# Optimization experiments

Hardware: AMD Instinct MI355X
Metric: run time of the kernel (lower is better)

## Reference

```python
import jax, jax.numpy as jnp
import numpy as np

N = 50000      # nodes
E = 800000     # edges
IN = 128       # in_dim
H = 8          # heads
C = 16         # h_dim (per-head out channels)
ED = 16        # edge_dim
G = 1000       # number of graphs
HC = H * C     # 128
EPS = 1e-16    # PyG softmax epsilon


def setup_inputs() -> dict:
    key = jax.random.key(0)
    ks = jax.random.split(key, 32)
    p = lambda i, shape: jax.random.normal(ks[i], shape, jnp.float32) * 0.1
    inp = {
        "x": jax.random.normal(ks[0], (N, IN), jnp.float32),
        "edge_index": jax.random.randint(ks[1], (2, E), 0, N),
        "edge_attr": jax.random.normal(ks[2], (E, ED), jnp.float32),
        "batch": jnp.sort(jax.random.randint(ks[3], (N,), 0, G)),
    }
    dims = [IN, HC, HC]
    for l in range(3):
        d = dims[l]
        inp[f"W{l+1}"] = p(4 + 6 * l, (d, HC))     # lin weight
        inp[f"We{l+1}"] = p(5 + 6 * l, (ED, HC))   # lin_edge weight
        inp[f"as{l+1}"] = p(6 + 6 * l, (H, C))     # att_src
        inp[f"ad{l+1}"] = p(7 + 6 * l, (H, C))     # att_dst
        inp[f"ae{l+1}"] = p(8 + 6 * l, (H, C))     # att_edge
        inp[f"b{l+1}"] = jnp.zeros((HC,), jnp.float32)
    D = 4 * HC  # cat(h1,h2,h3,h_pool_) -> 512
    inp["Wl1"] = p(22, (D, D)); inp["bl1"] = jnp.zeros((D,), jnp.float32)
    inp["Wl2"] = p(23, (D, 1)); inp["bl2"] = jnp.zeros((1,), jnp.float32)
    return inp


def gat_conv(x, src, dst, edge_attr, W, We, a_s, a_d, a_e, b):
    # x: [N, d_in] -> xs: [N, H, C]
    xs = (x @ W).reshape(-1, H, C)
    ea = (edge_attr @ We).reshape(-1, H, C)          # [E, H, C]
    al_src = jnp.sum(xs * a_s, axis=-1)              # [N, H]
    al_dst = jnp.sum(xs * a_d, axis=-1)              # [N, H]
    al_e = jnp.sum(ea * a_e, axis=-1)                # [E, H]
    alpha = al_src[src] + al_dst[dst] + al_e         # [E, H]
    alpha = jax.nn.leaky_relu(alpha, 0.2)
    amax = jax.ops.segment_max(alpha, dst, num_segments=N)
    ex = jnp.exp(alpha - amax[dst])
    denom = jax.ops.segment_sum(ex, dst, num_segments=N)
    alpha = ex / (denom[dst] + EPS)                  # softmax over in-edges of dst
    msg = xs[src] * alpha[..., None]                 # [E, H, C]
    out = jax.ops.segment_sum(msg, dst, num_segments=N)  # [N, H, C]
    return out.reshape(-1, HC) + b


def reference(x, edge_index, edge_attr, batch,
              W1, We1, as1, ad1, ae1, b1,
              W2, We2, as2, ad2, ae2, b2,
              W3, We3, as3, ad3, ae3, b3,
              Wl1, bl1, Wl2, bl2):
    src, dst = edge_index[0], edge_index[1]
    h1 = gat_conv(x, src, dst, edge_attr, W1, We1, as1, ad1, ae1, b1)
    h2 = gat_conv(h1, src, dst, edge_attr, W2, We2, as2, ad2, ae2, b2)
    h3 = gat_conv(h2, src, dst, edge_attr, W3, We3, as3, ad3, ae3, b3)
    # global_add_pool then broadcast back per node (vectorized gather,
    # replacing the original per-node python loop)
    h_pool = jax.ops.segment_sum(h3, batch, num_segments=G)   # [G, HC]
    h_pool_ = h_pool[batch]                                    # [N, HC]
    h = jnp.concatenate([h1, h2, h3, h_pool_], axis=1)         # [N, 4*HC]
    h = jax.nn.leaky_relu(h @ Wl1 + bl1, 0.01)
    return h @ Wl2 + bl2
```

## Files before the change

### kernel.cpp

```cpp
#include <hip/hip_runtime.h>

#define N_NODES 50000
#define N_EDGES 800000
#define N_GRAPH 1000
#define EPAD (N_EDGES + 8 * N_NODES)

typedef short bf16x8 __attribute__((ext_vector_type(8)));
typedef float f32x4 __attribute__((ext_vector_type(4)));

__device__ inline short f2b(float f) {
    union { float f; unsigned u; } x; x.f = f;
    unsigned r = x.u + 0x7FFF + ((x.u >> 16) & 1);
    return (short)(r >> 16);
}
__device__ inline float b2f_lo(unsigned v) {
    union { unsigned u; float f; } x; x.u = v << 16; return x.f;
}
__device__ inline float b2f_hi(unsigned v) {
    union { unsigned u; float f; } x; x.u = v & 0xFFFF0000u; return x.f;
}
__device__ inline float b2f_s(short s) {
    union { unsigned u; float f; } x; x.u = ((unsigned)(unsigned short)s) << 16; return x.f;
}
__device__ inline unsigned pack2(short lo, short hi) {
    return ((unsigned)(unsigned short)lo) | (((unsigned)(unsigned short)hi) << 16);
}

__global__ void f2b_bulk(const float* __restrict__ in, short* __restrict__ out, int n4) {
    int t = blockIdx.x * blockDim.x + threadIdx.x;
    if (t >= n4) return;
    float4 v = *(const float4*)(in + (size_t)t * 4);
    *(short4*)(out + (size_t)t * 4) = make_short4(f2b(v.x), f2b(v.y), f2b(v.z), f2b(v.w));
}

__global__ void wbt_k(const float* __restrict__ W, short* __restrict__ WbT) {
    int idx = blockIdx.x * blockDim.x + threadIdx.x;
    int k = idx >> 7, c = idx & 127;
    WbT[(size_t)c * 128 + k] = f2b(W[idx]);
}

__global__ __launch_bounds__(256) void gemm_mfma(const short* __restrict__ Ab,
                                                 const short* __restrict__ WbT,
                                                 short* __restrict__ outb, int nrows) {
    const int tid = threadIdx.x;
    const int n0 = blockIdx.x * 64;
    const int wid = tid >> 6, lane = tid & 63;
    const int lr = lane & 15, kg = lane >> 4;
    const int wr = (wid >> 1) * 32;
    const int wc = (wid & 1) * 64;

    f32x4 acc[2][4] = {};

#pragma unroll
    for (int ks = 0; ks < 4; ks++) {
        const int k0 = ks * 32;
        bf16x8 a[2], b[4];
#pragma unroll
        for (int fm = 0; fm < 2; fm++) {
            int gr = n0 + wr + fm * 16 + lr;
            bf16x8 v = {};
            if (gr < nrows) v = *(const bf16x8*)(Ab + (size_t)gr * 128 + k0 + kg * 8);
            a[fm] = v;
        }
#pragma unroll
        for (int fn = 0; fn < 4; fn++)
            b[fn] = *(const bf16x8*)(WbT + (size_t)(wc + fn * 16 + lr) * 128 + k0 + kg * 8);
#pragma unroll
        for (int fm = 0; fm < 2; fm++)
#pragma unroll
            for (int fn = 0; fn < 4; fn++)
                acc[fm][fn] = __builtin_amdgcn_mfma_f32_16x16x32_bf16(
                    a[fm], b[fn], acc[fm][fn], 0, 0, 0);
    }
#pragma unroll
    for (int fm = 0; fm < 2; fm++) {
#pragma unroll
        for (int r = 0; r < 4; r++) {
            int gr = n0 + wr + fm * 16 + kg * 4 + r;
            if (gr < nrows) {
#pragma unroll
                for (int fn = 0; fn < 4; fn++) {
                    int col = wc + fn * 16 + lr;
                    outb[(size_t)gr * 128 + col] = f2b(acc[fm][fn][r]);
                }
            }
        }
    }
}

__global__ void node_al(const short* __restrict__ xsb, const float* __restrict__ a_s,
                        const float* __restrict__ a_d, float* __restrict__ alsrc,
                        float* __restrict__ aldst, int n) {
    int t = blockIdx.x * blockDim.x + threadIdx.x;
    if (t >= n * 8) return;
    int node = t >> 3, h = t & 7;
    const short* xp = xsb + (size_t)node * 128 + h * 16;
    uint4 u0 = *(const uint4*)(xp);
    uint4 u1 = *(const uint4*)(xp + 8);
    unsigned w[8] = {u0.x, u0.y, u0.z, u0.w, u1.x, u1.y, u1.z, u1.w};
    float ss = 0.f, dd = 0.f;
#pragma unroll
    for (int q = 0; q < 8; q++) {
        float lo = b2f_lo(w[q]), hi = b2f_hi(w[q]);
        ss += lo * a_s[h * 16 + q * 2] + hi * a_s[h * 16 + q * 2 + 1];
        dd += lo * a_d[h * 16 + q * 2] + hi * a_d[h * 16 + q * 2 + 1];
    }
    alsrc[t] = ss;
    aldst[t] = dd;
}

__global__ void hist_k(const int* __restrict__ ei, int* __restrict__ cnt, int ne) {
    int e = blockIdx.x * blockDim.x + threadIdx.x;
    if (e < ne) atomicAdd(&cnt[ei[ne + e]], 1);
}

__global__ void scan1_k(const int* __restrict__ cnt, int* __restrict__ rowptr,
                        int* __restrict__ part, int n) {
    __shared__ int s[256];
    int tid = threadIdx.x;
    int i = blockIdx.x * 256 + tid;
    int v = (i < n) ? ((cnt[i] + 7) & ~7) : 0;
    s[tid] = v; __syncthreads();
#pragma unroll
    for (int off = 1; off < 256; off <<= 1) {
        int t = (tid >= off) ? s[tid - off] : 0;
        __syncthreads();
        s[tid] += t;
        __syncthreads();
    }
    if (i < n) rowptr[i] = s[tid] - v;
    if (tid == 255) part[blockIdx.x] = s[255];
}

__global__ void scan2_k(int* __restrict__ part, int npart) {
    __shared__ int s[256];
    int tid = threadIdx.x;
    int v = (tid < npart) ? part[tid] : 0;
    s[tid] = v; __syncthreads();
#pragma unroll
    for (int off = 1; off < 256; off <<= 1) {
        int t = (tid >= off) ? s[tid - off] : 0;
        __syncthreads();
        s[tid] += t;
        __syncthreads();
    }
    if (tid < npart) part[tid] = s[tid] - v;
}

__global__ void scan3_k(int* __restrict__ rowptr, const int* __restrict__ part,
                        const int* __restrict__ cnt, int* __restrict__ cursor, int n) {
    int i = blockIdx.x * 256 + threadIdx.x;
    if (i < n) {
        int r = rowptr[i] + part[blockIdx.x];
        rowptr[i] = r;
        cursor[i] = r;
        if (i == n - 1) rowptr[n] = r + ((cnt[i] + 7) & ~7);
    }
}

__global__ void scatter_k(const int* __restrict__ ei, const float* __restrict__ eattr,
                          int* __restrict__ cursor, int* __restrict__ csr_src,
                          short* __restrict__ eatb, int ne) {
    int e = blockIdx.x * blockDim.x + threadIdx.x;
    if (e >= ne) return;
    int d = ei[ne + e];
    int p = atomicAdd(&cursor[d], 1);
    csr_src[p] = ei[e];
    const float4* ep = (const float4*)(eattr + (size_t)e * 16);
    short* op = eatb + (size_t)p * 16;
#pragma unroll
    for (int q = 0; q < 4; q++) {
        float4 v = ep[q];
        *(short4*)(op + q * 4) = make_short4(f2b(v.x), f2b(v.y), f2b(v.z), f2b(v.w));
    }
}

__global__ __launch_bounds__(256) void ale_k(const int* __restrict__ csr_src,
                                             const short* __restrict__ eatb,
                                             const float* __restrict__ alsrc,
                                             const float* __restrict__ We,
                                             const float* __restrict__ ae,
                                             short* __restrict__ aleb, int ntot) {
    __shared__ float sAe[128];
    if (threadIdx.x < 128) {
        int k = threadIdx.x >> 3, h = threadIdx.x & 7;
        float s = 0.f;
#pragma unroll
        for (int c = 0; c < 16; c++) s += We[k * 128 + h * 16 + c] * ae[h * 16 + c];
        sAe[threadIdx.x] = s;
    }
    __syncthreads();
    int e = blockIdx.x * blockDim.x + threadIdx.x;
    if (e >= ntot) return;
    int s = csr_src[e];
    short* op = aleb + (size_t)e * 8;
    if (s < 0) {
        short m = f2b(-300.f);
        *(short4*)(op)     = make_short4(m, m, m, m);
        *(short4*)(op + 4) = make_short4(m, m, m, m);
        return;
    }
    uint4 u0 = *(const uint4*)(eatb + (size_t)e * 16);
    uint4 u1 = *(const uint4*)(eatb + (size_t)e * 16 + 8);
    unsigned w[8] = {u0.x, u0.y, u0.z, u0.w, u1.x, u1.y, u1.z, u1.w};
    float ea[16];
#pragma unroll
    for (int q = 0; q < 8; q++) { ea[q * 2] = b2f_lo(w[q]); ea[q * 2 + 1] = b2f_hi(w[q]); }
    float out[8];
    const float4* ap = (const float4*)(alsrc + (size_t)s * 8);
    float4 a0 = ap[0], a1 = ap[1];
    out[0] = a0.x; out[1] = a0.y; out[2] = a0.z; out[3] = a0.w;
    out[4] = a1.x; out[5] = a1.y; out[6] = a1.z; out[7] = a1.w;
#pragma unroll
    for (int k = 0; k < 16; k++)
#pragma unroll
        for (int h = 0; h < 8; h++) out[h] += ea[k] * sAe[k * 8 + h];
    short v8[8];
#pragma unroll
    for (int h = 0; h < 8; h++) v8[h] = f2b(out[h]);
    *(short4*)(op)     = make_short4(v8[0], v8[1], v8[2], v8[3]);
    *(short4*)(op + 4) = make_short4(v8[4], v8[5], v8[6], v8[7]);
}

__global__ __launch_bounds__(256) void gather_k(const int* __restrict__ rowptr,
                                                const int* __restrict__ csr_src,
                                                const short* __restrict__ aleb,
                                                const float* __restrict__ aldst,
                                                const short* __restrict__ xsb,
                                                const float* __restrict__ b,
                                                short* __restrict__ houtb, int n) {
    int dst = blockIdx.x * 4 + (threadIdx.x >> 6);
    if (dst >= n) return;
    const int lane = threadIdx.x & 63;
    const int h = lane >> 3;
    const float L2E = 1.44269504f;
    int p0 = rowptr[dst], p1 = rowptr[dst + 1];
    float ald = aldst[dst * 8 + h];
    float den = 0.f, acc0 = 0.f, acc1 = 0.f;
    const int nfull = (p1 - p0) >> 3;
    int p = p0;
    int   sv  = 0;
    float alv = 0.f;
    if (nfull > 0) {
        sv  = csr_src[p + (lane & 7)];
        alv = b2f_s(aleb[(size_t)p * 8 + lane]);
    }
    for (int c = 0; c < nfull; c++) {
        int csv = sv; float calv = alv;
        int pn = p + 8;
        if (c + 1 < nfull) {
            sv  = csr_src[pn + (lane & 7)];
            alv = b2f_s(aleb[(size_t)pn * 8 + lane]);
        }
        int s0 = __shfl(csv, 0), s1 = __shfl(csv, 1), s2 = __shfl(csv, 2), s3 = __shfl(csv, 3);
        int s4 = __shfl(csv, 4), s5 = __shfl(csv, 5), s6 = __shfl(csv, 6), s7 = __shfl(csv, 7);
        s0 = s0 < 0 ? 0 : s0;  s1 = s1 < 0 ? 0 : s1;
        s2 = s2 < 0 ? 0 : s2;  s3 = s3 < 0 ? 0 : s3;
        s4 = s4 < 0 ? 0 : s4;  s5 = s5 < 0 ? 0 : s5;
        s6 = s6 < 0 ? 0 : s6;  s7 = s7 < 0 ? 0 : s7;
        unsigned v0 = *(const unsigned*)(xsb + (size_t)s0 * 128 + lane * 2);
        unsigned v1 = *(const unsigned*)(xsb + (size_t)s1 * 128 + lane * 2);
        unsigned v2 = *(const unsigned*)(xsb + (size_t)s2 * 128 + lane * 2);
        unsigned v3 = *(const unsigned*)(xsb + (size_t)s3 * 128 + lane * 2);
        unsigned v4 = *(const unsigned*)(xsb + (size_t)s4 * 128 + lane * 2);
        unsigned v5 = *(const unsigned*)(xsb + (size_t)s5 * 128 + lane * 2);
        unsigned v6 = *(const unsigned*)(xsb + (size_t)s6 * 128 + lane * 2);
        unsigned v7 = *(const unsigned*)(xsb + (size_t)s7 * 128 + lane * 2);
        unsigned vv[8] = {v0, v1, v2, v3, v4, v5, v6, v7};
#pragma unroll
        for (int i = 0; i < 8; i++) {
            float al = __shfl(calv, i * 8 + h);
            float lg = al + ald; lg = lg > 0.f ? lg : 0.2f * lg;
            float ex = exp2f(lg * L2E);
            den  += ex;
            acc0 += b2f_lo(vv[i]) * ex;
            acc1 += b2f_hi(vv[i]) * ex;
        }
        p = pn;
    }
    float inv = 1.f / (den + 1e-16f);
    const float2 bb = *(const float2*)(b + lane * 2);
    unsigned o = pack2(f2b(acc0 * inv + bb.x), f2b(acc1 * inv + bb.y));
    *(unsigned*)(houtb + (size_t)dst * 128 + lane * 2) = o;
}

__global__ void pool_k(const short* __restrict__ h3b, const int* __restrict__ batch,
                       float* __restrict__ pool, int n) {
    int t = blockIdx.x * blockDim.x + threadIdx.x;
    if (t >= n * 128) return;
    int node = t >> 7, j = t & 127;
    atomicAdd(pool + (size_t)batch[node] * 128 + j, b2f_s(h3b[t]));
}

__global__ void wl1t_k(const float* __restrict__ Wl1, short* __restrict__ Wl1T) {
    int idx = blockIdx.x * blockDim.x + threadIdx.x;
    int k = idx >> 9, c = idx & 511;
    Wl1T[(size_t)c * 512 + k] = f2b(Wl1[idx]);
}

__global__ void init_out(float* __restrict__ out, const float* __restrict__ bl2, int n) {
    int t = blockIdx.x * blockDim.x + threadIdx.x;
    if (t < n) out[t] = bl2[0];
}

__global__ __launch_bounds__(256) void final_mfma(
    const short* __restrict__ h1, const short* __restrict__ h2,
    const short* __restrict__ h3, const short* __restrict__ poolb,
    const int* __restrict__ batch, const short* __restrict__ Wl1T,
    const float* __restrict__ bl1, const float* __restrict__ Wl2,
    float* __restrict__ out, int nrows)
{
    __shared__ short Abuf[2][4 * 64 * 8];
    __shared__ int   sBatch[64];
    const int tid = threadIdx.x;
    const int n0 = blockIdx.x * 64;
    const int j0 = blockIdx.y * 256;
    const int wid = tid >> 6, lane = tid & 63;
    const int lr = lane & 15, kg = lane >> 4;

    if (tid < 64) {
        int gr = n0 + tid;
        sBatch[tid] = (gr < nrows) ? batch[gr] : 0;
    }
    __syncthreads();

    const short* seg_base[4] = {h1, h2, h3, poolb};

    auto STAGE = [&](int t) {
        const int k0 = t * 32;
        const int seg = k0 >> 7;
        const short* base = seg_base[seg];
        const int cseg = k0 & 127;
        int gr = n0 + lane;
        int grow = (seg == 3) ? sBatch[lane] : ((gr < nrows) ? gr : 0);
        const short* src = base + (size_t)grow * 128 + cseg + wid * 8;
#if __has_builtin(__builtin_amdgcn_global_load_lds)
        __builtin_amdgcn_global_load_lds(
            (const __attribute__((address_space(1))) unsigned int*)src,
            (__attribute__((address_space(3))) unsigned int*)&Abuf[t & 1][(wid * 64 + lane) * 8],
            16, 0, 0);
#else
        uint4 v = *(const uint4*)src;
        *(uint4*)(&Abuf[t & 1][(wid * 64 + lane) * 8]) = v;
#endif
    };
    auto LOADB = [&](int t, bf16x8* bb) {
        const int k0 = t * 32;
#pragma unroll
        for (int fn = 0; fn < 4; fn++)
            bb[fn] = *(const bf16x8*)(Wl1T + (size_t)(j0 + wid * 64 + fn * 16 + lr) * 512
                                      + k0 + kg * 8);
    };

    f32x4 acc[4][4] = {};
    bf16x8 bc[4], bn[4];

    STAGE(0);
    LOADB(0, bc);
    __syncthreads();
#pragma unroll
    for (int t = 0; t < 16; t++) {
        if (t < 15) {
            STAGE(t + 1);
            LOADB(t + 1, bn);
        }
        bf16x8 a[4];
#pragma unroll
        for (int fm = 0; fm < 4; fm++)
            a[fm] = *(const bf16x8*)(&Abuf[t & 1][(kg * 64 + fm * 16 + lr) * 8]);
#pragma unroll
        for (int fm = 0; fm < 4; fm++)
#pragma unroll
            for (int fn = 0; fn < 4; fn++)
                acc[fm][fn] = __builtin_amdgcn_mfma_f32_16x16x32_bf16(
                    a[fm], bc[fn], acc[fm][fn], 0, 0, 0);
        if (t < 15) {
            __syncthreads();
#pragma unroll
            for (int fn = 0; fn < 4; fn++) bc[fn] = bn[fn];
        }
    }

    float w2[4], b1c[4];
#pragma unroll
    for (int fn = 0; fn < 4; fn++) {
        int c = j0 + wid * 64 + fn * 16 + lr;
        w2[fn]  = Wl2[c];
        b1c[fn] = bl1[c];
    }

#pragma unroll
    for (int fm = 0; fm < 4; fm++) {
#pragma unroll
        for (int r = 0; r < 4; r++) {
            float s = 0.f;
#pragma unroll
            for (int fn = 0; fn < 4; fn++) {
                float z = acc[fm][fn][r] + b1c[fn];
                z = z > 0.f ? z : 0.01f * z;
                s += z * w2[fn];
            }
            s += __shfl_xor(s, 1);
            s += __shfl_xor(s, 2);
            s += __shfl_xor(s, 4);
            s += __shfl_xor(s, 8);
            if (lr == 0) {
                int gr = n0 + fm * 16 + kg * 4 + r;
                if (gr < nrows) atomicAdd(out + gr, s);
            }
        }
    }
}

extern "C" void kernel_launch(void* const* d_in, const int* in_sizes, int n_in,
                              void* d_out, int out_size, void* d_ws, size_t ws_size,
                              hipStream_t stream) {
    const float* x     = (const float*)d_in[0];
    const int*   ei    = (const int*)d_in[1];
    const float* eattr = (const float*)d_in[2];
    const int*   batch = (const int*)d_in[3];
    const float* W[3]   = {(const float*)d_in[4],  (const float*)d_in[10], (const float*)d_in[16]};
    const float* We[3]  = {(const float*)d_in[5],  (const float*)d_in[11], (const float*)d_in[17]};
    const float* as_[3] = {(const float*)d_in[6],  (const float*)d_in[12], (const float*)d_in[18]};
    const float* ad_[3] = {(const float*)d_in[7],  (const float*)d_in[13], (const float*)d_in[19]};
    const float* ae_[3] = {(const float*)d_in[8],  (const float*)d_in[14], (const float*)d_in[20]};
    const float* b_[3]  = {(const float*)d_in[9],  (const float*)d_in[15], (const float*)d_in[21]};
    const float* Wl1 = (const float*)d_in[22];
    const float* bl1 = (const float*)d_in[23];
    const float* Wl2 = (const float*)d_in[24];
    const float* bl2 = (const float*)d_in[25];

    const int N = N_NODES, E = N_EDGES, G = N_GRAPH;

    float* ws    = (float*)d_ws;
    float* alsrc = ws;
    float* aldst = alsrc + (size_t)N * 8;
    float* pool  = aldst + (size_t)N * 8;
    short* xb    = (short*)(pool + (size_t)G * 128);
    short* xsb   = xb + (size_t)N * 128;
    short* hb0   = xsb + (size_t)N * 128;
    short* hb1   = hb0 + (size_t)N * 128;
    short* hb2   = hb1 + (size_t)N * 128;
    short* hb[3] = {hb0, hb1, hb2};
    short* poolb = hb2 + (size_t)N * 128;
    short* wbt0  = poolb + (size_t)G * 128;
    short* wbt1  = wbt0 + 16384;
    short* wbt2  = wbt1 + 16384;
    short* wbt[3] = {wbt0, wbt1, wbt2};
    short* wl1t  = wbt2 + 16384;
    short* aleb  = wl1t + 262144;
    short* eatb  = aleb + (size_t)EPAD * 8;
    int*   cnt     = (int*)(eatb + (size_t)EPAD * 16);
    int*   rowptr  = cnt + N;
    int*   cursor  = rowptr + N + 1;
    int*   part    = cursor + N;
    int*   csr_src = part + 256;

    f2b_bulk<<<(N * 32 + 255) / 256, 256, 0, stream>>>(x, xb, N * 32);
    for (int l = 0; l < 3; l++)
        wbt_k<<<64, 256, 0, stream>>>(W[l], wbt[l]);
    wl1t_k<<<1024, 256, 0, stream>>>(Wl1, wl1t);
    hipMemsetAsync(cnt, 0, (size_t)N * sizeof(int), stream);
    hipMemsetAsync(csr_src, 0x80, (size_t)EPAD * sizeof(int), stream);
    hist_k<<<(E + 255) / 256, 256, 0, stream>>>(ei, cnt, E);
    const int nblk = (N + 255) / 256;
    scan1_k<<<nblk, 256, 0, stream>>>(cnt, rowptr, part, N);
    scan2_k<<<1, 256, 0, stream>>>(part, nblk);
    scan3_k<<<nblk, 256, 0, stream>>>(rowptr, part, cnt, cursor, N);
    scatter_k<<<(E + 255) / 256, 256, 0, stream>>>(ei, eattr, cursor, csr_src, eatb, E);

    const int aleGrid = (EPAD + 255) / 256;
    for (int l = 0; l < 3; l++) {
        const short* Ain = (l == 0) ? xb : hb[l - 1];
        gemm_mfma<<<(N + 63) / 64, 256, 0, stream>>>(Ain, wbt[l], xsb, N);
        node_al<<<(N * 8 + 255) / 256, 256, 0, stream>>>(xsb, as_[l], ad_[l], alsrc, aldst, N);
        ale_k<<<aleGrid, 256, 0, stream>>>(csr_src, eatb, alsrc, We[l], ae_[l], aleb, EPAD);
        gather_k<<<(N + 3) / 4, 256, 0, stream>>>(rowptr, csr_src, aleb, aldst, xsb,
                                                  b_[l], hb[l], N);
    }
    hipMemsetAsync(pool, 0, (size_t)G * 128 * sizeof(float), stream);
    pool_k<<<(N * 128 + 255) / 256, 256, 0, stream>>>(hb[2], batch, pool, N);
    f2b_bulk<<<(G * 32 + 255) / 256, 256, 0, stream>>>(pool, poolb, G * 32);

    init_out<<<(N + 255) / 256, 256, 0, stream>>>((float*)d_out, bl2, N);
    dim3 fg((N + 63) / 64, 2);
    final_mfma<<<fg, 256, 0, stream>>>(hb[0], hb[1], hb[2], poolb, batch,
                                       wl1t, bl1, Wl2, (float*)d_out, N);
}
```

Baseline: 453.7 us.

## Fuse edge attention logits into gather and replace atomic pooling with segmented reduction

Drops the separate per-edge ale_k pass, which wrote bf16 edge logits to memory each layer. gather_k now computes them inline from the bf16 edge attributes, src logits and a precomputed We·ae projection that a new aew3_k builds once for all three layers. Global add pooling moves from per-element float atomics plus a conversion kernel to one block per graph, which reads graph boundaries derived from the sorted batch vector. This cuts edge-sized memory traffic and atomics, but adds shuffle and ALU work to the gather loop and relies on batch being sorted.

```diff
diff --git a/kernel.cpp b/kernel.cpp
--- a/kernel.cpp
+++ b/kernel.cpp
@@ -37,6 +37,20 @@
     int idx = blockIdx.x * blockDim.x + threadIdx.x;
     int k = idx >> 7, c = idx & 127;
     WbT[(size_t)c * 128 + k] = f2b(W[idx]);
+}
+
+__global__ void aew3_k(const float* __restrict__ We0, const float* __restrict__ ae0,
+                       const float* __restrict__ We1, const float* __restrict__ ae1,
+                       const float* __restrict__ We2, const float* __restrict__ ae2,
+                       float* __restrict__ aeW3) {
+    const float* We = (blockIdx.x == 0) ? We0 : (blockIdx.x == 1) ? We1 : We2;
+    const float* ae = (blockIdx.x == 0) ? ae0 : (blockIdx.x == 1) ? ae1 : ae2;
+    int t = threadIdx.x;
+    int k = t >> 3, h = t & 7;
+    float s = 0.f;
+#pragma unroll
+    for (int c = 0; c < 16; c++) s += We[k * 128 + h * 16 + c] * ae[h * 16 + c];
+    aeW3[blockIdx.x * 128 + t] = s;
 }
 
 __global__ __launch_bounds__(256) void gemm_mfma(const short* __restrict__ Ab,
@@ -175,101 +189,93 @@
     }
 }
 
-__global__ __launch_bounds__(256) void ale_k(const int* __restrict__ csr_src,
-                                             const short* __restrict__ eatb,
-                                             const float* __restrict__ alsrc,
-                                             const float* __restrict__ We,
-                                             const float* __restrict__ ae,
-                                             short* __restrict__ aleb, int ntot) {
-    __shared__ float sAe[128];
-    if (threadIdx.x < 128) {
-        int k = threadIdx.x >> 3, h = threadIdx.x & 7;
-        float s = 0.f;
-#pragma unroll
-        for (int c = 0; c < 16; c++) s += We[k * 128 + h * 16 + c] * ae[h * 16 + c];
-        sAe[threadIdx.x] = s;
-    }
+__global__ void gbound_k(const int* __restrict__ batch, int* __restrict__ gb, int n, int g) {
+    int i = blockIdx.x * 256 + threadIdx.x;
+    if (i >= n) return;
+    int b1 = batch[i];
+    int b0 = (i == 0) ? -1 : batch[i - 1];
+    for (int q = b0 + 1; q <= b1; q++) gb[q] = i;
+    if (i == n - 1)
+        for (int q = b1 + 1; q <= g; q++) gb[q] = n;
+}
+
+__global__ __launch_bounds__(256) void pools_k(const short* __restrict__ h3b,
+                                               const int* __restrict__ gb,
+                                               short* __restrict__ poolb) {
+    __shared__ float red[128];
+    int g = blockIdx.x;
+    int c = threadIdx.x & 127;
+    int par = threadIdx.x >> 7;
+    int i0 = gb[g], i1 = gb[g + 1];
+    float s = 0.f;
+    for (int i = i0 + par; i < i1; i += 2) s += b2f_s(h3b[(size_t)i * 128 + c]);
+    if (par == 1) red[c] = s;
     __syncthreads();
-    int e = blockIdx.x * blockDim.x + threadIdx.x;
-    if (e >= ntot) return;
-    int s = csr_src[e];
-    short* op = aleb + (size_t)e * 8;
-    if (s < 0) {
-        short m = f2b(-300.f);
-        *(short4*)(op)     = make_short4(m, m, m, m);
-        *(short4*)(op + 4) = make_short4(m, m, m, m);
-        return;
-    }
-    uint4 u0 = *(const uint4*)(eatb + (size_t)e * 16);
-    uint4 u1 = *(const uint4*)(eatb + (size_t)e * 16 + 8);
-    unsigned w[8] = {u0.x, u0.y, u0.z, u0.w, u1.x, u1.y, u1.z, u1.w};
-    float ea[16];
-#pragma unroll
-    for (int q = 0; q < 8; q++) { ea[q * 2] = b2f_lo(w[q]); ea[q * 2 + 1] = b2f_hi(w[q]); }
-    float out[8];
-    const float4* ap = (const float4*)(alsrc + (size_t)s * 8);
-    float4 a0 = ap[0], a1 = ap[1];
-    out[0] = a0.x; out[1] = a0.y; out[2] = a0.z; out[3] = a0.w;
-    out[4] = a1.x; out[5] = a1.y; out[6] = a1.z; out[7] = a1.w;
-#pragma unroll
-    for (int k = 0; k < 16; k++)
-#pragma unroll
-        for (int h = 0; h < 8; h++) out[h] += ea[k] * sAe[k * 8 + h];
-    short v8[8];
-#pragma unroll
-    for (int h = 0; h < 8; h++) v8[h] = f2b(out[h]);
-    *(short4*)(op)     = make_short4(v8[0], v8[1], v8[2], v8[3]);
-    *(short4*)(op + 4) = make_short4(v8[4], v8[5], v8[6], v8[7]);
+    if (par == 0) poolb[(size_t)g * 128 + c] = f2b(s + red[c]);
 }
 
 __global__ __launch_bounds__(256) void gather_k(const int* __restrict__ rowptr,
                                                 const int* __restrict__ csr_src,
-                                                const short* __restrict__ aleb,
+                                                const short* __restrict__ eatb,
+                                                const float* __restrict__ aeW,
+                                                const float* __restrict__ alsrc,
                                                 const float* __restrict__ aldst,
                                                 const short* __restrict__ xsb,
                                                 const float* __restrict__ b,
                                                 short* __restrict__ houtb, int n) {
+    __shared__ float sAe[128];
+    if (threadIdx.x < 128) sAe[threadIdx.x] = aeW[threadIdx.x];
+    __syncthreads();
     int dst = blockIdx.x * 4 + (threadIdx.x >> 6);
     if (dst >= n) return;
     const int lane = threadIdx.x & 63;
-    const int h = lane >> 3;
+    const int h  = lane >> 3;
+    const int pe = lane >> 3;
+    const int ph = lane & 7;
     const float L2E = 1.44269504f;
     int p0 = rowptr[dst], p1 = rowptr[dst + 1];
     float ald = aldst[dst * 8 + h];
     float den = 0.f, acc0 = 0.f, acc1 = 0.f;
     const int nfull = (p1 - p0) >> 3;
     int p = p0;
-    int   sv  = 0;
-    float alv = 0.f;
+    int svo = 0; unsigned w = 0;
     if (nfull > 0) {
-        sv  = csr_src[p + (lane & 7)];
-        alv = b2f_s(aleb[(size_t)p * 8 + lane]);
+        svo = csr_src[p + pe];
+        w = *(const unsigned*)(eatb + (size_t)(p + pe) * 16 + ph * 2);
     }
     for (int c = 0; c < nfull; c++) {
-        int csv = sv; float calv = alv;
+        int csv = svo; unsigned cw = w;
         int pn = p + 8;
         if (c + 1 < nfull) {
-            sv  = csr_src[pn + (lane & 7)];
-            alv = b2f_s(aleb[(size_t)pn * 8 + lane]);
-        }
-        int s0 = __shfl(csv, 0), s1 = __shfl(csv, 1), s2 = __shfl(csv, 2), s3 = __shfl(csv, 3);
-        int s4 = __shfl(csv, 4), s5 = __shfl(csv, 5), s6 = __shfl(csv, 6), s7 = __shfl(csv, 7);
-        s0 = s0 < 0 ? 0 : s0;  s1 = s1 < 0 ? 0 : s1;
-        s2 = s2 < 0 ? 0 : s2;  s3 = s3 < 0 ? 0 : s3;
-        s4 = s4 < 0 ? 0 : s4;  s5 = s5 < 0 ? 0 : s5;
-        s6 = s6 < 0 ? 0 : s6;  s7 = s7 < 0 ? 0 : s7;
-        unsigned v0 = *(const unsigned*)(xsb + (size_t)s0 * 128 + lane * 2);
-        unsigned v1 = *(const unsigned*)(xsb + (size_t)s1 * 128 + lane * 2);
-        unsigned v2 = *(const unsigned*)(xsb + (size_t)s2 * 128 + lane * 2);
-        unsigned v3 = *(const unsigned*)(xsb + (size_t)s3 * 128 + lane * 2);
-        unsigned v4 = *(const unsigned*)(xsb + (size_t)s4 * 128 + lane * 2);
-        unsigned v5 = *(const unsigned*)(xsb + (size_t)s5 * 128 + lane * 2);
-        unsigned v6 = *(const unsigned*)(xsb + (size_t)s6 * 128 + lane * 2);
-        unsigned v7 = *(const unsigned*)(xsb + (size_t)s7 * 128 + lane * 2);
+            svo = csr_src[pn + pe];
+            w = *(const unsigned*)(eatb + (size_t)(pn + pe) * 16 + ph * 2);
+        }
+        int sc = csv < 0 ? 0 : csv;
+        float pal = alsrc[sc * 8 + ph];
+#pragma unroll
+        for (int k = 0; k < 8; k++) {
+            unsigned u = __shfl(cw, pe * 8 + k);
+            pal += b2f_lo(u) * sAe[k * 16 + ph] + b2f_hi(u) * sAe[k * 16 + 8 + ph];
+        }
+        if (csv < 0) pal = -300.f;
+        int t0 = __shfl(csv, 0),  t1 = __shfl(csv, 8),  t2 = __shfl(csv, 16), t3 = __shfl(csv, 24);
+        int t4 = __shfl(csv, 32), t5 = __shfl(csv, 40), t6 = __shfl(csv, 48), t7 = __shfl(csv, 56);
+        t0 = t0 < 0 ? 0 : t0;  t1 = t1 < 0 ? 0 : t1;
+        t2 = t2 < 0 ? 0 : t2;  t3 = t3 < 0 ? 0 : t3;
+        t4 = t4 < 0 ? 0 : t4;  t5 = t5 < 0 ? 0 : t5;
+        t6 = t6 < 0 ? 0 : t6;  t7 = t7 < 0 ? 0 : t7;
+        unsigned v0 = *(const unsigned*)(xsb + (size_t)t0 * 128 + lane * 2);
+        unsigned v1 = *(const unsigned*)(xsb + (size_t)t1 * 128 + lane * 2);
+        unsigned v2 = *(const unsigned*)(xsb + (size_t)t2 * 128 + lane * 2);
+        unsigned v3 = *(const unsigned*)(xsb + (size_t)t3 * 128 + lane * 2);
+        unsigned v4 = *(const unsigned*)(xsb + (size_t)t4 * 128 + lane * 2);
+        unsigned v5 = *(const unsigned*)(xsb + (size_t)t5 * 128 + lane * 2);
+        unsigned v6 = *(const unsigned*)(xsb + (size_t)t6 * 128 + lane * 2);
+        unsigned v7 = *(const unsigned*)(xsb + (size_t)t7 * 128 + lane * 2);
         unsigned vv[8] = {v0, v1, v2, v3, v4, v5, v6, v7};
 #pragma unroll
         for (int i = 0; i < 8; i++) {
-            float al = __shfl(calv, i * 8 + h);
+            float al = __shfl(pal, i * 8 + h);
             float lg = al + ald; lg = lg > 0.f ? lg : 0.2f * lg;
             float ex = exp2f(lg * L2E);
             den  += ex;
@@ -282,14 +288,6 @@
     const float2 bb = *(const float2*)(b + lane * 2);
     unsigned o = pack2(f2b(acc0 * inv + bb.x), f2b(acc1 * inv + bb.y));
     *(unsigned*)(houtb + (size_t)dst * 128 + lane * 2) = o;
-}
-
-__global__ void pool_k(const short* __restrict__ h3b, const int* __restrict__ batch,
-                       float* __restrict__ pool, int n) {
-    int t = blockIdx.x * blockDim.x + threadIdx.x;
-    if (t >= n * 128) return;
-    int node = t >> 7, j = t & 127;
-    atomicAdd(pool + (size_t)batch[node] * 128 + j, b2f_s(h3b[t]));
 }
 
 __global__ void wl1t_k(const float* __restrict__ Wl1, short* __restrict__ Wl1T) {
@@ -435,8 +433,8 @@
     float* ws    = (float*)d_ws;
     float* alsrc = ws;
     float* aldst = alsrc + (size_t)N * 8;
-    float* pool  = aldst + (size_t)N * 8;
-    short* xb    = (short*)(pool + (size_t)G * 128);
+    float* aeW3  = aldst + (size_t)N * 8;
+    short* xb    = (short*)(aeW3 + 384);
     short* xsb   = xb + (size_t)N * 128;
     short* hb0   = xsb + (size_t)N * 128;
     short* hb1   = hb0 + (size_t)N * 128;
@@ -448,18 +446,19 @@
     short* wbt2  = wbt1 + 16384;
     short* wbt[3] = {wbt0, wbt1, wbt2};
     short* wl1t  = wbt2 + 16384;
-    short* aleb  = wl1t + 262144;
-    short* eatb  = aleb + (size_t)EPAD * 8;
+    short* eatb  = wl1t + 262144;
     int*   cnt     = (int*)(eatb + (size_t)EPAD * 16);
     int*   rowptr  = cnt + N;
     int*   cursor  = rowptr + N + 1;
     int*   part    = cursor + N;
-    int*   csr_src = part + 256;
+    int*   gb      = part + 256;
+    int*   csr_src = gb + G + 1;
 
     f2b_bulk<<<(N * 32 + 255) / 256, 256, 0, stream>>>(x, xb, N * 32);
     for (int l = 0; l < 3; l++)
         wbt_k<<<64, 256, 0, stream>>>(W[l], wbt[l]);
     wl1t_k<<<1024, 256, 0, stream>>>(Wl1, wl1t);
+    aew3_k<<<3, 128, 0, stream>>>(We[0], ae_[0], We[1], ae_[1], We[2], ae_[2], aeW3);
     hipMemsetAsync(cnt, 0, (size_t)N * sizeof(int), stream);
     hipMemsetAsync(csr_src, 0x80, (size_t)EPAD * sizeof(int), stream);
     hist_k<<<(E + 255) / 256, 256, 0, stream>>>(ei, cnt, E);
@@ -468,19 +467,16 @@
     scan2_k<<<1, 256, 0, stream>>>(part, nblk);
     scan3_k<<<nblk, 256, 0, stream>>>(rowptr, part, cnt, cursor, N);
     scatter_k<<<(E + 255) / 256, 256, 0, stream>>>(ei, eattr, cursor, csr_src, eatb, E);
-
-    const int aleGrid = (EPAD + 255) / 256;
+    gbound_k<<<nblk, 256, 0, stream>>>(batch, gb, N, G);
+
     for (int l = 0; l < 3; l++) {
         const short* Ain = (l == 0) ? xb : hb[l - 1];
         gemm_mfma<<<(N + 63) / 64, 256, 0, stream>>>(Ain, wbt[l], xsb, N);
         node_al<<<(N * 8 + 255) / 256, 256, 0, stream>>>(xsb, as_[l], ad_[l], alsrc, aldst, N);
-        ale_k<<<aleGrid, 256, 0, stream>>>(csr_src, eatb, alsrc, We[l], ae_[l], aleb, EPAD);
-        gather_k<<<(N + 3) / 4, 256, 0, stream>>>(rowptr, csr_src, aleb, aldst, xsb,
-                                                  b_[l], hb[l], N);
-    }
-    hipMemsetAsync(pool, 0, (size_t)G * 128 * sizeof(float), stream);
-    pool_k<<<(N * 128 + 255) / 256, 256, 0, stream>>>(hb[2], batch, pool, N);
-    f2b_bulk<<<(G * 32 + 255) / 256, 256, 0, stream>>>(pool, poolb, G * 32);
+        gather_k<<<(N + 3) / 4, 256, 0, stream>>>(rowptr, csr_src, eatb, aeW3 + l * 128,
+                                                  alsrc, aldst, xsb, b_[l], hb[l], N);
+    }
+    pools_k<<<G, 256, 0, stream>>>(hb[2], gb, poolb);
 
     init_out<<<(N + 255) / 256, 256, 0, stream>>>((float*)d_out, bl2, N);
     dim3 fg((N + 63) / 64, 2);
```

Result: faster. 435.3 us (-4.1%).
